# Kernel optimization log

Hardware: AMD Instinct MI355X
Metric: run time of the kernel (lower is better)

## Reference

```python
import jax, jax.numpy as jnp
import numpy as np


def _lstm_step(h, c, x, W_ih, W_hh, b_ih, b_hh):
    # PyTorch gate order: i, f, g, o
    gates = x @ W_ih.T + b_ih + h @ W_hh.T + b_hh
    i, f, g, o = jnp.split(gates, 4, axis=-1)
    c = jax.nn.sigmoid(f) * c + jax.nn.sigmoid(i) * jnp.tanh(g)
    h = jax.nn.sigmoid(o) * jnp.tanh(c)
    return h, c


def setup_inputs() -> dict:
    key = jax.random.key(0)
    ks = jax.random.split(key, 12)
    B, T = 256, 256
    S, A, H, K = 64, 16, 512, 512
    D = S + A  # 80
    s = 1.0 / np.sqrt(H)
    u = lambda k, shape, sc: jax.random.uniform(k, shape, jnp.float32, -sc, sc)
    return {
        "traj": jax.random.normal(ks[0], (B, T, D), jnp.float32),
        "seq_len": T,
        "enc_W_ih": u(ks[1], (4 * H, D), s),
        "enc_W_hh": u(ks[2], (4 * H, H), s),
        "enc_b_ih": u(ks[3], (4 * H,), s),
        "enc_b_hh": u(ks[4], (4 * H,), s),
        "embeddings": jax.random.uniform(ks[5], (K, H), jnp.float32, -1.0 / K, 1.0 / K),
        "dec_W_ih": u(ks[6], (4 * H, D), s),
        "dec_W_hh": u(ks[7], (4 * H, H), s),
        "dec_b_ih": u(ks[8], (4 * H,), s),
        "dec_b_hh": u(ks[9], (4 * H,), s),
        "fc_W": u(ks[10], (D, H), s),
        "fc_b": u(ks[11], (D,), s),
    }


def reference(traj, seq_len, enc_W_ih, enc_W_hh, enc_b_ih, enc_b_hh,
              embeddings, dec_W_ih, dec_W_hh, dec_b_ih, dec_b_hh, fc_W, fc_b):
    B = traj.shape[0]
    H = enc_W_hh.shape[1]
    D = traj.shape[-1]

    # ---- Encoder: many-to-one LSTM, keep final hidden state ----
    def enc_step(carry, x_t):
        h, c = carry
        h, c = _lstm_step(h, c, x_t, enc_W_ih, enc_W_hh, enc_b_ih, enc_b_hh)
        return (h, c), None
    h0 = jnp.zeros((B, H), traj.dtype)
    (z, _), _ = jax.lax.scan(enc_step, (h0, h0), jnp.swapaxes(traj, 0, 1))

    # ---- Vector quantizer ----
    d = (jnp.sum(z * z, axis=1, keepdims=True)
         + jnp.sum(embeddings * embeddings, axis=1)
         - 2.0 * z @ embeddings.T)  # [B, K]
    idx = jnp.argmin(d, axis=1)
    quantized = embeddings[idx]  # [B, H]
    e_latent = jnp.mean((jax.lax.stop_gradient(quantized) - z) ** 2)
    q_latent = jnp.mean((quantized - jax.lax.stop_gradient(z)) ** 2)
    vq_loss = q_latent + 0.25 * e_latent

    def dec_step(carry, _):
        h, c, x = carry
        h, c = _lstm_step(h, c, x, dec_W_ih, dec_W_hh, dec_b_ih, dec_b_hh)
        y = h @ fc_W.T + fc_b
        return (h, c, y), y
    x0 = jnp.zeros((B, D), traj.dtype)
    c0 = jnp.zeros((B, H), traj.dtype)
    _, ys = jax.lax.scan(dec_step, (quantized, c0, x0), None, length=seq_len)
    recon = jnp.swapaxes(ys, 0, 1)  # [B, seq_len, D]
    return recon, vq_loss, idx[:, None]
```

## Files before the change

kernel.cpp:

```cpp
#include <hip/hip_runtime.h>
#include <math.h>

#define BB 256
#define TT 256
#define DDIM 80
#define HDIM 512
#define ROWSTRIDE 20480

#define WS_HA    0
#define WS_CD    131072
#define WS_BAR   262144
#define WS_HB    263168
#define WS_QUANT 394240
#define WS_VQP   525312
#define WS_BENC  525568
#define WS_BDEC0 527616
#define WS_BEFF  529664
#define WS_WEFF  531712

typedef _Float16 f16;
typedef f16 half4_t __attribute__((ext_vector_type(4)));
typedef f16 half8_t __attribute__((ext_vector_type(8)));
typedef float float4_t __attribute__((ext_vector_type(4)));

__device__ __forceinline__ float sigmoid_fast(float v) {
  return __builtin_amdgcn_rcpf(1.0f + __builtin_amdgcn_exp2f(-1.44269504f * v));
}
__device__ __forceinline__ float tanh_fast(float v) {
  return 2.0f * __builtin_amdgcn_rcpf(1.0f + __builtin_amdgcn_exp2f(-2.88539008f * v)) - 1.0f;
}

__device__ __forceinline__ void llc_store_f32(float* p, float v) {
  asm volatile("global_store_dword %0, %1, off sc0 sc1" :: "v"(p), "v"(v) : "memory");
}
__device__ __forceinline__ void llc_store_i32(int* p, int v) {
  asm volatile("global_store_dword %0, %1, off sc0 sc1" :: "v"(p), "v"(v) : "memory");
}
__device__ __forceinline__ void wait_vm0() {
  asm volatile("s_waitcnt vmcnt(0)" ::: "memory");
}

__device__ __forceinline__ void poll_flag4(const int* fp, int done) {
  int a0, a1, a2, a3;
  asm volatile(
      "global_load_dword %0, %4, off sc0 sc1\n\t"
      "global_load_dword %1, %4, off sc0 sc1\n\t"
      "global_load_dword %2, %4, off sc0 sc1\n\t"
      "Lpoll%=:\n\t"
      "global_load_dword %3, %4, off sc0 sc1\n\t"
      "s_waitcnt vmcnt(3)\n\t"
      "v_cmp_gt_i32 vcc, %5, %0\n\t"
      "s_cbranch_vccz Ldone%=\n\t"
      "global_load_dword %0, %4, off sc0 sc1\n\t"
      "s_waitcnt vmcnt(3)\n\t"
      "v_cmp_gt_i32 vcc, %5, %1\n\t"
      "s_cbranch_vccz Ldone%=\n\t"
      "global_load_dword %1, %4, off sc0 sc1\n\t"
      "s_waitcnt vmcnt(3)\n\t"
      "v_cmp_gt_i32 vcc, %5, %2\n\t"
      "s_cbranch_vccz Ldone%=\n\t"
      "global_load_dword %2, %4, off sc0 sc1\n\t"
      "s_waitcnt vmcnt(3)\n\t"
      "v_cmp_gt_i32 vcc, %5, %3\n\t"
      "s_cbranch_vccnz Lpoll%=\n\t"
      "Ldone%=:\n\t"
      "s_waitcnt vmcnt(0)"
      : "=&v"(a0), "=&v"(a1), "=&v"(a2), "=&v"(a3)
      : "v"(fp), "s"(done)
      : "vcc", "memory");
}

__device__ __forceinline__ void llc_load_4xf4_cols(
    const float4* base,
    float4& a0, float4& a1, float4& a2, float4& a3) {
  asm volatile(
      "global_load_dwordx4 %0, %4, off sc0 sc1\n\t"
      "global_load_dwordx4 %1, %5, off sc0 sc1\n\t"
      "global_load_dwordx4 %2, %6, off sc0 sc1\n\t"
      "global_load_dwordx4 %3, %7, off sc0 sc1\n\t"
      "s_waitcnt vmcnt(0)"
      : "=&v"(a0), "=&v"(a1), "=&v"(a2), "=&v"(a3)
      : "v"(base), "v"(base + 32), "v"(base + 64), "v"(base + 96)
      : "memory");
}

__global__ __launch_bounds__(256) void zero_kernel(float4* __restrict__ p, int n4) {
  int i = blockIdx.x * 256 + threadIdx.x;
  if (i < n4) p[i] = make_float4(0.f, 0.f, 0.f, 0.f);
}

__global__ __launch_bounds__(256) void bias_init_kernel(
    const float* __restrict__ eb1, const float* __restrict__ eb2,
    const float* __restrict__ db1, const float* __restrict__ db2,
    const float* __restrict__ dWih, const float* __restrict__ fcb,
    float* __restrict__ b_enc, float* __restrict__ b_dec0,
    float* __restrict__ b_eff) {
  int n = blockIdx.x * 256 + threadIdx.x;
  b_enc[n] = eb1[n] + eb2[n];
  float bd = db1[n] + db2[n];
  b_dec0[n] = bd;
  float acc = bd;
  #pragma unroll 16
  for (int d = 0; d < DDIM; d++) acc += dWih[n * DDIM + d] * fcb[d];
  b_eff[n] = acc;
}

__global__ __launch_bounds__(256) void fold_kernel(
    const float* __restrict__ dWih, const float* __restrict__ dWhh,
    const float* __restrict__ fcW, float* __restrict__ W_eff) {
  int n = blockIdx.x;
  int tid = threadIdx.x;
  __shared__ float sw[DDIM];
  if (tid < DDIM) sw[tid] = dWih[n * DDIM + tid];
  __syncthreads();
  for (int k = tid; k < HDIM; k += 256) {
    float acc = dWhh[n * HDIM + k];
    #pragma unroll 16
    for (int d = 0; d < DDIM; d++) acc += sw[d] * fcW[d * HDIM + k];
    W_eff[n * HDIM + k] = acc;
  }
}

__global__ __launch_bounds__(256) void lstm_step_kernel(
    const float* __restrict__ Whh, const float* __restrict__ bias,
    const float* __restrict__ h_in, float* __restrict__ c,
    float* __restrict__ h_out) {
  __shared__ float sh[16][516];
  int tid = threadIdx.x;
  int rt = blockIdx.x & 15, jt = blockIdx.x >> 4;
  int row0 = rt << 4;
  for (int i = tid; i < 2048; i += 256) {
    int r = i >> 7, kq = i & 127;
    float4 v = *(const float4*)(h_in + (size_t)(row0 + r) * HDIM + (kq << 2));
    *(float4*)&sh[r][kq << 2] = v;
  }
  __syncthreads();
  int r = tid & 15, j0 = tid >> 4;
  int j = (jt << 4) + j0;
  float a0 = bias[j], a1 = bias[512 + j], a2 = bias[1024 + j], a3 = bias[1536 + j];
  const float4* w0 = (const float4*)(Whh + (size_t)j * HDIM);
  const float4* w1 = (const float4*)(Whh + (size_t)(512 + j) * HDIM);
  const float4* w2 = (const float4*)(Whh + (size_t)(1024 + j) * HDIM);
  const float4* w3 = (const float4*)(Whh + (size_t)(1536 + j) * HDIM);
  const float4* hv = (const float4*)&sh[r][0];
  #pragma unroll 4
  for (int kq = 0; kq < 128; kq++) {
    float4 h4 = hv[kq];
    float4 q0 = w0[kq], q1 = w1[kq], q2 = w2[kq], q3 = w3[kq];
    a0 += h4.x * q0.x + h4.y * q0.y + h4.z * q0.z + h4.w * q0.w;
    a1 += h4.x * q1.x + h4.y * q1.y + h4.z * q1.z + h4.w * q1.w;
    a2 += h4.x * q2.x + h4.y * q2.y + h4.z * q2.z + h4.w * q2.w;
    a3 += h4.x * q3.x + h4.y * q3.y + h4.z * q3.z + h4.w * q3.w;
  }
  size_t idx = (size_t)(row0 + r) * HDIM + j;
  float cv = c[idx];
  float cn = sigmoid_fast(a1) * cv + sigmoid_fast(a0) * tanh_fast(a2);
  float hn = sigmoid_fast(a3) * tanh_fast(cn);
  c[idx] = cn;
  h_out[idx] = hn;
}

template <int IS_DEC>
__global__ __launch_bounds__(512, 2) void lstm_persist(
    const float* __restrict__ W,
    const float* __restrict__ Wih,
    const float* __restrict__ bias,
    const float* __restrict__ traj,
    const float* __restrict__ c_init,
    const float* __restrict__ fcW, const float* __restrict__ fcb,
    float* __restrict__ recon,
    float* __restrict__ hA, float* __restrict__ hB,
    int* __restrict__ flags) {
  constexpr int KT  = IS_DEC ? 16 : 19;
  constexpr int AST = IS_DEC ? 520 : 616;
  constexpr int RST = 132;
  __shared__ f16 Ahi[16 * AST];
  __shared__ f16 Alo[16 * AST];
  __shared__ float red[16 * RST];
  __shared__ float ypart[IS_DEC ? 8 * 260 : 4];

  const int tid = threadIdx.x;
  const int bid = blockIdx.x;
  const int rt = bid & 15, jt = bid >> 4;
  const int r0 = rt * 16, d0 = jt * 32;
  const int wv = __builtin_amdgcn_readfirstlane(tid >> 6);
  const int l15 = tid & 15;
  const int q = (tid >> 4) & 3;
  const int dh = wv >> 2, nt = wv & 3;

  #define SPLITC(vv, k) { \
    int off = (tid >> 5) * AST + (((tid & 31) + (k) * 32) << 2); \
    half4_t hi4, lo4; \
    float f0 = vv.x, f1 = vv.y, f2 = vv.z, f3 = vv.w; \
    f16 a = (f16)f0, b = (f16)f1, cc = (f16)f2, d = (f16)f3; \
    hi4[0] = a; hi4[1] = b; hi4[2] = cc; hi4[3] = d; \
    lo4[0] = (f16)(f0 - (float)a); lo4[1] = (f16)(f1 - (float)b); \
    lo4[2] = (f16)(f2 - (float)cc); lo4[3] = (f16)(f3 - (float)d); \
    *(half4_t*)&Ahi[off] = hi4; *(half4_t*)&Alo[off] = lo4; }

  const int grow = nt * 512 + d0 + dh * 16 + l15;
  half8_t Whi[KT], Wlo[KT];
  #pragma unroll
  for (int kt = 0; kt < KT; kt++) {
    #pragma unroll
    for (int j = 0; j < 8; j++) {
      int k = kt * 32 + q * 8 + j;
      float w;
      if (k < 512) w = W[(size_t)grow * HDIM + k];
      else {
        int kx = k - 512;
        w = (!IS_DEC && kx < DDIM) ? Wih[(size_t)grow * DDIM + kx] : 0.f;
      }
      f16 hi = (f16)w;
      Whi[kt][j] = hi;
      Wlo[kt][j] = (f16)(w - (float)hi);
    }
  }
  const float breg = bias[grow];

  half8_t Fhi[2], Flo[2];
  float ybias = 0.f;
  if (IS_DEC && jt < 5) {
    const int drow = jt * 16 + l15;
    #pragma unroll
    for (int kk = 0; kk < 2; kk++) {
      const int kt = wv * 2 + kk;
      #pragma unroll
      for (int j = 0; j < 8; j++) {
        float w = fcW[(size_t)drow * HDIM + kt * 32 + q * 8 + j];
        f16 hi = (f16)w;
        Fhi[kk][j] = hi;
        Flo[kk][j] = (f16)(w - (float)hi);
      }
    }
    ybias = fcb[jt * 16 + l15];
  }

  const int eb = tid >> 5, ed = tid & 31;
  float c_reg = IS_DEC ? c_init[(size_t)(r0 + eb) * HDIM + d0 + ed] : 0.f;
  __syncthreads();

  #define MFMA_RANGE(LO, HI) { \
    _Pragma("unroll") \
    for (int kt = (LO); kt < (HI); kt++) { \
      half8_t ahi = *(const half8_t*)&Ahi[abase + kt * 32]; \
      half8_t alo = *(const half8_t*)&Alo[abase + kt * 32]; \
      if (kt & 1) { \
        acc1 = __builtin_amdgcn_mfma_f32_16x16x32_f16(ahi, Whi[kt], acc1, 0, 0, 0); \
        acc1 = __builtin_amdgcn_mfma_f32_16x16x32_f16(alo, Whi[kt], acc1, 0, 0, 0); \
        acc1 = __builtin_amdgcn_mfma_f32_16x16x32_f16(ahi, Wlo[kt], acc1, 0, 0, 0); \
        acc1 = __builtin_amdgcn_mfma_f32_16x16x32_f16(alo, Wlo[kt], acc1, 0, 0, 0); \
      } else { \
        acc0 = __builtin_amdgcn_mfma_f32_16x16x32_f16(ahi, Whi[kt], acc0, 0, 0, 0); \
        acc0 = __builtin_amdgcn_mfma_f32_16x16x32_f16(alo, Whi[kt], acc0, 0, 0, 0); \
        acc0 = __builtin_amdgcn_mfma_f32_16x16x32_f16(ahi, Wlo[kt], acc0, 0, 0, 0); \
        acc0 = __builtin_amdgcn_mfma_f32_16x16x32_f16(alo, Wlo[kt], acc0, 0, 0, 0); \
      } \
    } }

  const int t_begin = IS_DEC ? 1 : 0;
  for (int t = t_begin; t < TT; t++) {
    const float* hin = (t & 1) ? hB : hA;
    float* hout = (t & 1) ? hA : hB;

    float4 xv0;
    if (!IS_DEC && tid < 384) {
      int row = tid / 24, c4 = tid % 24;
      xv0 = (c4 < 20)
          ? *(const float4*)(traj + (size_t)(r0 + row) * ROWSTRIDE +
                             (size_t)t * DDIM + c4 * 4)
          : make_float4(0.f, 0.f, 0.f, 0.f);
    }

    float4 v0, v1, v2, v3;
    const float4* base =
        (const float4*)(hin + (size_t)r0 * HDIM) + (tid >> 5) * 128 + (tid & 31);
    const bool is_t0 = (!IS_DEC && t == 0);
    if (!is_t0) {
      asm volatile(
          "global_load_dwordx4 %0, %4, off sc0 sc1\n\t"
          "global_load_dwordx4 %1, %5, off sc0 sc1\n\t"
          "global_load_dwordx4 %2, %6, off sc0 sc1\n\t"
          "global_load_dwordx4 %3, %7, off sc0 sc1"
          : "=&v"(v0), "=&v"(v1), "=&v"(v2), "=&v"(v3)
          : "v"(base), "v"(base + 32), "v"(base + 64), "v"(base + 96)
          : "memory");
      asm volatile("s_waitcnt vmcnt(2)" ::: "memory");
      __builtin_amdgcn_sched_barrier(0);
      SPLITC(v0, 0); SPLITC(v1, 1);
    } else {
      const int fo = (tid >> 5) * AST + ((tid & 31) << 4);
      uint4 z4; z4.x = 0; z4.y = 0; z4.z = 0; z4.w = 0;
      *(uint4*)&Ahi[fo] = z4; *(uint4*)&Ahi[fo + 8] = z4;
      *(uint4*)&Alo[fo] = z4; *(uint4*)&Alo[fo + 8] = z4;
    }
    __syncthreads();

    float4_t acc0 = {breg, breg, breg, breg};
    float4_t acc1 = {0.f, 0.f, 0.f, 0.f};
    const int abase = l15 * AST + q * 8;
    MFMA_RANGE(0, 8);

    if (!is_t0) {
      asm volatile("s_waitcnt vmcnt(0)" ::: "memory");
      __builtin_amdgcn_sched_barrier(0);
      SPLITC(v2, 2); SPLITC(v3, 3);
    }
    if (!IS_DEC && tid < 384) {
      int row = tid / 24, c4 = tid % 24;
      int off = row * AST + 512 + c4 * 4;
      half4_t hi4, lo4;
      float f0 = xv0.x, f1 = xv0.y, f2 = xv0.z, f3 = xv0.w;
      f16 a = (f16)f0, b = (f16)f1, cc = (f16)f2, d = (f16)f3;
      hi4[0] = a; hi4[1] = b; hi4[2] = cc; hi4[3] = d;
      lo4[0] = (f16)(f0 - (float)a); lo4[1] = (f16)(f1 - (float)b);
      lo4[2] = (f16)(f2 - (float)cc); lo4[3] = (f16)(f3 - (float)d);
      *(half4_t*)&Ahi[off] = hi4; *(half4_t*)&Alo[off] = lo4;
    }
    __syncthreads();
    MFMA_RANGE(8, KT);
    {
      float4_t C = acc0 + acc1;
      #pragma unroll
      for (int i = 0; i < 4; i++)
        red[(q * 4 + i) * RST + nt * 32 + dh * 16 + l15] = C[i];
    }
    __syncthreads();

    {
      float ig = red[eb * RST + ed];
      float fg = red[eb * RST + 32 + ed];
      float gg = red[eb * RST + 64 + ed];
      float og = red[eb * RST + 96 + ed];
      float cn = sigmoid_fast(fg) * c_reg + sigmoid_fast(ig) * tanh_fast(gg);
      c_reg = cn;
      llc_store_f32(&hout[(size_t)(r0 + eb) * HDIM + d0 + ed],
                    sigmoid_fast(og) * tanh_fast(cn));
    }
    wait_vm0();
    __syncthreads();

    const int done = t - t_begin + 1;
    const bool do_bar = IS_DEC || t < TT - 1;
    if (do_bar && tid == 0) llc_store_i32(&flags[rt * 16 + jt], done);

    if (IS_DEC && jt < 5) {
      float4_t ya = {0.f, 0.f, 0.f, 0.f};
      #pragma unroll
      for (int kk = 0; kk < 2; kk++) {
        const int kt = wv * 2 + kk;
        const int ao = l15 * AST + kt * 32 + q * 8;
        half8_t ahi = *(const half8_t*)&Ahi[ao];
        half8_t alo = *(const half8_t*)&Alo[ao];
        ya = __builtin_amdgcn_mfma_f32_16x16x32_f16(ahi, Fhi[kk], ya, 0, 0, 0);
        ya = __builtin_amdgcn_mfma_f32_16x16x32_f16(alo, Fhi[kk], ya, 0, 0, 0);
        ya = __builtin_amdgcn_mfma_f32_16x16x32_f16(ahi, Flo[kk], ya, 0, 0, 0);
        ya = __builtin_amdgcn_mfma_f32_16x16x32_f16(alo, Flo[kk], ya, 0, 0, 0);
      }
      #pragma unroll
      for (int i = 0; i < 4; i++)
        ypart[wv * 260 + (q * 4 + i) * 16 + l15] = ya[i];
      __syncthreads();
      if (tid < 256) {
        float acc = ybias;
        #pragma unroll
        for (int w8 = 0; w8 < 8; w8++) acc += ypart[w8 * 260 + tid];
        recon[(size_t)(r0 + (tid >> 4)) * ROWSTRIDE + (size_t)(t - 1) * DDIM +
              jt * 16 + (tid & 15)] = acc;
      }
    }

    if (do_bar) {
      if (tid < 64) poll_flag4(flags + rt * 16 + (tid & 15), done);
      __syncthreads();
    }
  }

  if (IS_DEC) {
    if (jt >= 5) return;
    {
      const float4* base =
          (const float4*)(hA + (size_t)r0 * HDIM) + (tid >> 5) * 128 + (tid & 31);
      float4 v0, v1, v2, v3;
      llc_load_4xf4_cols(base, v0, v1, v2, v3);
      __builtin_amdgcn_sched_barrier(0);
      SPLITC(v0, 0); SPLITC(v1, 1); SPLITC(v2, 2); SPLITC(v3, 3);
    }
    __syncthreads();
    {
      float4_t ya = {0.f, 0.f, 0.f, 0.f};
      #pragma unroll
      for (int kk = 0; kk < 2; kk++) {
        const int kt = wv * 2 + kk;
        const int ao = l15 * AST + kt * 32 + q * 8;
        half8_t ahi = *(const half8_t*)&Ahi[ao];
        half8_t alo = *(const half8_t*)&Alo[ao];
        ya = __builtin_amdgcn_mfma_f32_16x16x32_f16(ahi, Fhi[kk], ya, 0, 0, 0);
        ya = __builtin_amdgcn_mfma_f32_16x16x32_f16(alo, Fhi[kk], ya, 0, 0, 0);
        ya = __builtin_amdgcn_mfma_f32_16x16x32_f16(ahi, Flo[kk], ya, 0, 0, 0);
        ya = __builtin_amdgcn_mfma_f32_16x16x32_f16(alo, Flo[kk], ya, 0, 0, 0);
      }
      #pragma unroll
      for (int i = 0; i < 4; i++)
        ypart[wv * 260 + (q * 4 + i) * 16 + l15] = ya[i];
    }
    __syncthreads();
    if (tid < 256) {
      float acc = ybias;
      #pragma unroll
      for (int w8 = 0; w8 < 8; w8++) acc += ypart[w8 * 260 + tid];
      recon[(size_t)(r0 + (tid >> 4)) * ROWSTRIDE + (size_t)255 * DDIM +
            jt * 16 + (tid & 15)] = acc;
    }
  }
  #undef SPLITC
  #undef MFMA_RANGE
}

__global__ __launch_bounds__(256) void vq_kernel(
    const float* __restrict__ z, const float* __restrict__ emb,
    float* __restrict__ quant, float* __restrict__ vq_part,
    float* __restrict__ out_idx) {
  __shared__ float sz[512];
  __shared__ float sd[256];
  __shared__ int si[256];
  int b = blockIdx.x, tid = threadIdx.x;
  sz[tid] = z[(size_t)b * HDIM + tid];
  sz[tid + 256] = z[(size_t)b * HDIM + 256 + tid];
  __syncthreads();
  float bd = 3.4e38f;
  int bk = 0;
  for (int k = tid; k < 512; k += 256) {
    const float4* e4 = (const float4*)(emb + (size_t)k * HDIM);
    const float4* z4 = (const float4*)sz;
    float dot = 0.f, ee = 0.f;
    #pragma unroll 4
    for (int qq = 0; qq < 128; qq++) {
      float4 ev = e4[qq], zv = z4[qq];
      dot += ev.x * zv.x + ev.y * zv.y + ev.z * zv.z + ev.w * zv.w;
      ee += ev.x * ev.x + ev.y * ev.y + ev.z * ev.z + ev.w * ev.w;
    }
    float dist = ee - 2.f * dot;
    if (dist < bd) { bd = dist; bk = k; }
  }
  sd[tid] = bd; si[tid] = bk;
  __syncthreads();
  for (int s = 128; s > 0; s >>= 1) {
    if (tid < s) {
      float od = sd[tid + s]; int ok = si[tid + s];
      if (od < sd[tid] || (od == sd[tid] && ok < si[tid])) { sd[tid] = od; si[tid] = ok; }
    }
    __syncthreads();
  }
  int kbest = si[0];
  __syncthreads();
  float e0 = emb[(size_t)kbest * HDIM + tid];
  float e1 = emb[(size_t)kbest * HDIM + 256 + tid];
  quant[(size_t)b * HDIM + tid] = e0;
  quant[(size_t)b * HDIM + 256 + tid] = e1;
  float q0 = e0 - sz[tid], q1 = e1 - sz[tid + 256];
  sd[tid] = q0 * q0 + q1 * q1;
  __syncthreads();
  for (int st = 128; st > 0; st >>= 1) {
    if (tid < st) sd[tid] += sd[tid + st];
    __syncthreads();
  }
  if (tid == 0) { vq_part[b] = sd[0]; out_idx[b] = (float)kbest; }
}

__global__ __launch_bounds__(256) void vq_reduce_kernel(const float* __restrict__ vq_part,
                                                        float* __restrict__ out_loss) {
  __shared__ float s[256];
  int tid = threadIdx.x;
  s[tid] = vq_part[tid];
  __syncthreads();
  for (int st = 128; st > 0; st >>= 1) {
    if (tid < st) s[tid] += s[tid + st];
    __syncthreads();
  }
  if (tid == 0) out_loss[0] = s[0] * 1.25f / (float)(BB * HDIM);
}

extern "C" void kernel_launch(void* const* d_in, const int* in_sizes, int n_in,
                              void* d_out, int out_size, void* d_ws, size_t ws_size,
                              hipStream_t stream) {
  const float* traj = (const float*)d_in[0];
  const float* eWih = (const float*)d_in[2];
  const float* eWhh = (const float*)d_in[3];
  const float* eb1  = (const float*)d_in[4];
  const float* eb2  = (const float*)d_in[5];
  const float* emb  = (const float*)d_in[6];
  const float* dWih = (const float*)d_in[7];
  const float* dWhh = (const float*)d_in[8];
  const float* db1  = (const float*)d_in[9];
  const float* db2  = (const float*)d_in[10];
  const float* fcW  = (const float*)d_in[11];
  const float* fcb  = (const float*)d_in[12];

  float* out = (float*)d_out;
  float* recon = out;
  float* out_loss = out + 5242880;
  float* out_idx = out + 5242881;

  float* ws = (float*)d_ws;
  float* hA      = ws + WS_HA;
  float* cD      = ws + WS_CD;
  int*   bar     = (int*)(ws + WS_BAR);
  float* hB      = ws + WS_HB;
  float* quant   = ws + WS_QUANT;
  float* vq_part = ws + WS_VQP;
  float* b_enc   = ws + WS_BENC;
  float* b_dec0  = ws + WS_BDEC0;
  float* b_eff   = ws + WS_BEFF;
  float* W_eff   = ws + WS_WEFF;

  zero_kernel<<<257, 256, 0, stream>>>((float4*)ws, 65792);
  bias_init_kernel<<<8, 256, 0, stream>>>(eb1, eb2, db1, db2, dWih, fcb,
                                          b_enc, b_dec0, b_eff);
  fold_kernel<<<2048, 256, 0, stream>>>(dWih, dWhh, fcW, W_eff);

  lstm_persist<0><<<256, 512, 0, stream>>>(
      eWhh, eWih, b_enc, traj, nullptr, nullptr, nullptr, nullptr, hA, hB, bar);

  vq_kernel<<<256, 256, 0, stream>>>(hA, emb, quant, vq_part, out_idx);
  vq_reduce_kernel<<<1, 256, 0, stream>>>(vq_part, out_loss);

  lstm_step_kernel<<<512, 256, 0, stream>>>(dWhh, b_dec0, quant, cD, hB);
  lstm_persist<1><<<256, 512, 0, stream>>>(
      W_eff, nullptr, b_eff, nullptr, cD, fcW, fcb, recon, hA, hB, bar + 256);
}
```

Measured before the change: 1.973 ms.

## Double per-block hidden slice in persistent LSTM, halving blocks and barrier fan-in

The persistent encoder and decoder LSTM kernels are relaunched as 128 blocks of 1024 threads instead of 256 blocks of 512, so each block owns 64 hidden columns instead of 32. The h-tile staging, gate reduction buffer, fc projection split and flag layout are reworked to match, so each row group now synchronises 8 blocks per step instead of 16. This is meant to cut the cross-block barrier cost on each recurrent step. The risk is register pressure: 1024-thread blocks (and the aggressive launch bounds) limit per-thread registers, and spilling the register-resident weight tiles could outweigh the sync savings.

```diff
diff --git a/kernel.cpp b/kernel.cpp
--- a/kernel.cpp
+++ b/kernel.cpp
@@ -70,20 +70,6 @@
       : "vcc", "memory");
 }
 
-__device__ __forceinline__ void llc_load_4xf4_cols(
-    const float4* base,
-    float4& a0, float4& a1, float4& a2, float4& a3) {
-  asm volatile(
-      "global_load_dwordx4 %0, %4, off sc0 sc1\n\t"
-      "global_load_dwordx4 %1, %5, off sc0 sc1\n\t"
-      "global_load_dwordx4 %2, %6, off sc0 sc1\n\t"
-      "global_load_dwordx4 %3, %7, off sc0 sc1\n\t"
-      "s_waitcnt vmcnt(0)"
-      : "=&v"(a0), "=&v"(a1), "=&v"(a2), "=&v"(a3)
-      : "v"(base), "v"(base + 32), "v"(base + 64), "v"(base + 96)
-      : "memory");
-}
-
 __global__ __launch_bounds__(256) void zero_kernel(float4* __restrict__ p, int n4) {
   int i = blockIdx.x * 256 + threadIdx.x;
   if (i < n4) p[i] = make_float4(0.f, 0.f, 0.f, 0.f);
@@ -161,7 +147,7 @@
 }
 
 template <int IS_DEC>
-__global__ __launch_bounds__(512, 2) void lstm_persist(
+__global__ __launch_bounds__(1024, 4) void lstm_persist(
     const float* __restrict__ W,
     const float* __restrict__ Wih,
     const float* __restrict__ bias,
@@ -173,23 +159,23 @@
     int* __restrict__ flags) {
   constexpr int KT  = IS_DEC ? 16 : 19;
   constexpr int AST = IS_DEC ? 520 : 616;
-  constexpr int RST = 132;
+  constexpr int RST = 260;
   __shared__ f16 Ahi[16 * AST];
   __shared__ f16 Alo[16 * AST];
   __shared__ float red[16 * RST];
-  __shared__ float ypart[IS_DEC ? 8 * 260 : 4];
+  __shared__ float ypart[IS_DEC ? 16 * 260 : 4];
 
   const int tid = threadIdx.x;
   const int bid = blockIdx.x;
   const int rt = bid & 15, jt = bid >> 4;
-  const int r0 = rt * 16, d0 = jt * 32;
+  const int r0 = rt * 16, d0 = jt * 64;
   const int wv = __builtin_amdgcn_readfirstlane(tid >> 6);
   const int l15 = tid & 15;
   const int q = (tid >> 4) & 3;
-  const int dh = wv >> 2, nt = wv & 3;
+  const int nt = wv & 3, dq = wv >> 2;
 
   #define SPLITC(vv, k) { \
-    int off = (tid >> 5) * AST + (((tid & 31) + (k) * 32) << 2); \
+    int off = (tid >> 6) * AST + (((tid & 63) + (k) * 64) << 2); \
     half4_t hi4, lo4; \
     float f0 = vv.x, f1 = vv.y, f2 = vv.z, f3 = vv.w; \
     f16 a = (f16)f0, b = (f16)f1, cc = (f16)f2, d = (f16)f3; \
@@ -198,7 +184,7 @@
     lo4[2] = (f16)(f2 - (float)cc); lo4[3] = (f16)(f3 - (float)d); \
     *(half4_t*)&Ahi[off] = hi4; *(half4_t*)&Alo[off] = lo4; }
 
-  const int grow = nt * 512 + d0 + dh * 16 + l15;
+  const int grow = nt * 512 + d0 + dq * 16 + l15;
   half8_t Whi[KT], Wlo[KT];
   #pragma unroll
   for (int kt = 0; kt < KT; kt++) {
@@ -218,25 +204,21 @@
   }
   const float breg = bias[grow];
 
-  half8_t Fhi[2], Flo[2];
+  half8_t Fhi, Flo;
   float ybias = 0.f;
   if (IS_DEC && jt < 5) {
     const int drow = jt * 16 + l15;
     #pragma unroll
-    for (int kk = 0; kk < 2; kk++) {
-      const int kt = wv * 2 + kk;
-      #pragma unroll
-      for (int j = 0; j < 8; j++) {
-        float w = fcW[(size_t)drow * HDIM + kt * 32 + q * 8 + j];
-        f16 hi = (f16)w;
-        Fhi[kk][j] = hi;
-        Flo[kk][j] = (f16)(w - (float)hi);
-      }
+    for (int j = 0; j < 8; j++) {
+      float w = fcW[(size_t)drow * HDIM + wv * 32 + q * 8 + j];
+      f16 hi = (f16)w;
+      Fhi[j] = hi;
+      Flo[j] = (f16)(w - (float)hi);
     }
     ybias = fcb[jt * 16 + l15];
   }
 
-  const int eb = tid >> 5, ed = tid & 31;
+  const int eb = tid >> 6, ed = tid & 63;
   float c_reg = IS_DEC ? c_init[(size_t)(r0 + eb) * HDIM + d0 + ed] : 0.f;
   __syncthreads();
 
@@ -272,27 +254,25 @@
           : make_float4(0.f, 0.f, 0.f, 0.f);
     }
 
-    float4 v0, v1, v2, v3;
+    float4 v0, v1;
     const float4* base =
-        (const float4*)(hin + (size_t)r0 * HDIM) + (tid >> 5) * 128 + (tid & 31);
+        (const float4*)(hin + (size_t)r0 * HDIM) + (tid >> 6) * 128 + (tid & 63);
     const bool is_t0 = (!IS_DEC && t == 0);
     if (!is_t0) {
       asm volatile(
-          "global_load_dwordx4 %0, %4, off sc0 sc1\n\t"
-          "global_load_dwordx4 %1, %5, off sc0 sc1\n\t"
-          "global_load_dwordx4 %2, %6, off sc0 sc1\n\t"
-          "global_load_dwordx4 %3, %7, off sc0 sc1"
-          : "=&v"(v0), "=&v"(v1), "=&v"(v2), "=&v"(v3)
-          : "v"(base), "v"(base + 32), "v"(base + 64), "v"(base + 96)
+          "global_load_dwordx4 %0, %2, off sc0 sc1\n\t"
+          "global_load_dwordx4 %1, %3, off sc0 sc1"
+          : "=&v"(v0), "=&v"(v1)
+          : "v"(base), "v"(base + 64)
           : "memory");
-      asm volatile("s_waitcnt vmcnt(2)" ::: "memory");
+      asm volatile("s_waitcnt vmcnt(1)" ::: "memory");
       __builtin_amdgcn_sched_barrier(0);
-      SPLITC(v0, 0); SPLITC(v1, 1);
+      SPLITC(v0, 0);
     } else {
-      const int fo = (tid >> 5) * AST + ((tid & 31) << 4);
-      uint4 z4; z4.x = 0; z4.y = 0; z4.z = 0; z4.w = 0;
-      *(uint4*)&Ahi[fo] = z4; *(uint4*)&Ahi[fo + 8] = z4;
-      *(uint4*)&Alo[fo] = z4; *(uint4*)&Alo[fo + 8] = z4;
+      const int fo = (tid >> 6) * AST + ((tid & 63) << 2);
+      half4_t z4 = {(f16)0, (f16)0, (f16)0, (f16)0};
+      *(half4_t*)&Ahi[fo] = z4; *(half4_t*)&Ahi[fo + 256] = z4;
+      *(half4_t*)&Alo[fo] = z4; *(half4_t*)&Alo[fo + 256] = z4;
     }
     __syncthreads();
 
@@ -304,7 +284,7 @@
     if (!is_t0) {
       asm volatile("s_waitcnt vmcnt(0)" ::: "memory");
       __builtin_amdgcn_sched_barrier(0);
-      SPLITC(v2, 2); SPLITC(v3, 3);
+      SPLITC(v1, 1);
     }
     if (!IS_DEC && tid < 384) {
       int row = tid / 24, c4 = tid % 24;
@@ -323,15 +303,15 @@
       float4_t C = acc0 + acc1;
       #pragma unroll
       for (int i = 0; i < 4; i++)
-        red[(q * 4 + i) * RST + nt * 32 + dh * 16 + l15] = C[i];
+        red[(q * 4 + i) * RST + nt * 64 + dq * 16 + l15] = C[i];
     }
     __syncthreads();
 
     {
       float ig = red[eb * RST + ed];
-      float fg = red[eb * RST + 32 + ed];
-      float gg = red[eb * RST + 64 + ed];
-      float og = red[eb * RST + 96 + ed];
+      float fg = red[eb * RST + 64 + ed];
+      float gg = red[eb * RST + 128 + ed];
+      float og = red[eb * RST + 192 + ed];
       float cn = sigmoid_fast(fg) * c_reg + sigmoid_fast(ig) * tanh_fast(gg);
       c_reg = cn;
       llc_store_f32(&hout[(size_t)(r0 + eb) * HDIM + d0 + ed],
@@ -342,20 +322,18 @@
 
     const int done = t - t_begin + 1;
     const bool do_bar = IS_DEC || t < TT - 1;
-    if (do_bar && tid == 0) llc_store_i32(&flags[rt * 16 + jt], done);
+    if (do_bar && tid == 0) llc_store_i32(&flags[rt * 8 + jt], done);
 
     if (IS_DEC && jt < 5) {
       float4_t ya = {0.f, 0.f, 0.f, 0.f};
-      #pragma unroll
-      for (int kk = 0; kk < 2; kk++) {
-        const int kt = wv * 2 + kk;
-        const int ao = l15 * AST + kt * 32 + q * 8;
+      {
+        const int ao = l15 * AST + wv * 32 + q * 8;
         half8_t ahi = *(const half8_t*)&Ahi[ao];
         half8_t alo = *(const half8_t*)&Alo[ao];
-        ya = __builtin_amdgcn_mfma_f32_16x16x32_f16(ahi, Fhi[kk], ya, 0, 0, 0);
-        ya = __builtin_amdgcn_mfma_f32_16x16x32_f16(alo, Fhi[kk], ya, 0, 0, 0);
-        ya = __builtin_amdgcn_mfma_f32_16x16x32_f16(ahi, Flo[kk], ya, 0, 0, 0);
-        ya = __builtin_amdgcn_mfma_f32_16x16x32_f16(alo, Flo[kk], ya, 0, 0, 0);
+        ya = __builtin_amdgcn_mfma_f32_16x16x32_f16(ahi, Fhi, ya, 0, 0, 0);
+        ya = __builtin_amdgcn_mfma_f32_16x16x32_f16(alo, Fhi, ya, 0, 0, 0);
+        ya = __builtin_amdgcn_mfma_f32_16x16x32_f16(ahi, Flo, ya, 0, 0, 0);
+        ya = __builtin_amdgcn_mfma_f32_16x16x32_f16(alo, Flo, ya, 0, 0, 0);
       }
       #pragma unroll
       for (int i = 0; i < 4; i++)
@@ -364,14 +342,14 @@
       if (tid < 256) {
         float acc = ybias;
         #pragma unroll
-        for (int w8 = 0; w8 < 8; w8++) acc += ypart[w8 * 260 + tid];
+        for (int w16 = 0; w16 < 16; w16++) acc += ypart[w16 * 260 + tid];
         recon[(size_t)(r0 + (tid >> 4)) * ROWSTRIDE + (size_t)(t - 1) * DDIM +
               jt * 16 + (tid & 15)] = acc;
       }
     }
 
     if (do_bar) {
-      if (tid < 64) poll_flag4(flags + rt * 16 + (tid & 15), done);
+      if (tid < 64) poll_flag4(flags + rt * 8 + (tid & 7), done);
       __syncthreads();
     }
   }
@@ -380,25 +358,29 @@
     if (jt >= 5) return;
     {
       const float4* base =
-          (const float4*)(hA + (size_t)r0 * HDIM) + (tid >> 5) * 128 + (tid & 31);
-      float4 v0, v1, v2, v3;
-      llc_load_4xf4_cols(base, v0, v1, v2, v3);
+          (const float4*)(hA + (size_t)r0 * HDIM) + (tid >> 6) * 128 + (tid & 63);
+      float4 v0, v1;
+      asm volatile(
+          "global_load_dwordx4 %0, %2, off sc0 sc1\n\t"
+          "global_load_dwordx4 %1, %3, off sc0 sc1\n\t"
+          "s_waitcnt vmcnt(0)"
+          : "=&v"(v0), "=&v"(v1)
+          : "v"(base), "v"(base + 64)
+          : "memory");
       __builtin_amdgcn_sched_barrier(0);
-      SPLITC(v0, 0); SPLITC(v1, 1); SPLITC(v2, 2); SPLITC(v3, 3);
+      SPLITC(v0, 0); SPLITC(v1, 1);
     }
     __syncthreads();
     {
       float4_t ya = {0.f, 0.f, 0.f, 0.f};
-      #pragma unroll
-      for (int kk = 0; kk < 2; kk++) {
-        const int kt = wv * 2 + kk;
-        const int ao = l15 * AST + kt * 32 + q * 8;
+      {
+        const int ao = l15 * AST + wv * 32 + q * 8;
         half8_t ahi = *(const half8_t*)&Ahi[ao];
         half8_t alo = *(const half8_t*)&Alo[ao];
-        ya = __builtin_amdgcn_mfma_f32_16x16x32_f16(ahi, Fhi[kk], ya, 0, 0, 0);
-        ya = __builtin_amdgcn_mfma_f32_16x16x32_f16(alo, Fhi[kk], ya, 0, 0, 0);
-        ya = __builtin_amdgcn_mfma_f32_16x16x32_f16(ahi, Flo[kk], ya, 0, 0, 0);
-        ya = __builtin_amdgcn_mfma_f32_16x16x32_f16(alo, Flo[kk], ya, 0, 0, 0);
+        ya = __builtin_amdgcn_mfma_f32_16x16x32_f16(ahi, Fhi, ya, 0, 0, 0);
+        ya = __builtin_amdgcn_mfma_f32_16x16x32_f16(alo, Fhi, ya, 0, 0, 0);
+        ya = __builtin_amdgcn_mfma_f32_16x16x32_f16(ahi, Flo, ya, 0, 0, 0);
+        ya = __builtin_amdgcn_mfma_f32_16x16x32_f16(alo, Flo, ya, 0, 0, 0);
       }
       #pragma unroll
       for (int i = 0; i < 4; i++)
@@ -408,7 +390,7 @@
     if (tid < 256) {
       float acc = ybias;
       #pragma unroll
-      for (int w8 = 0; w8 < 8; w8++) acc += ypart[w8 * 260 + tid];
+      for (int w16 = 0; w16 < 16; w16++) acc += ypart[w16 * 260 + tid];
       recon[(size_t)(r0 + (tid >> 4)) * ROWSTRIDE + (size_t)255 * DDIM +
             jt * 16 + (tid & 15)] = acc;
     }
@@ -519,13 +501,13 @@
                                           b_enc, b_dec0, b_eff);
   fold_kernel<<<2048, 256, 0, stream>>>(dWih, dWhh, fcW, W_eff);
 
-  lstm_persist<0><<<256, 512, 0, stream>>>(
+  lstm_persist<0><<<128, 1024, 0, stream>>>(
       eWhh, eWih, b_enc, traj, nullptr, nullptr, nullptr, nullptr, hA, hB, bar);
 
   vq_kernel<<<256, 256, 0, stream>>>(hA, emb, quant, vq_part, out_idx);
   vq_reduce_kernel<<<1, 256, 0, stream>>>(vq_part, out_loss);
 
   lstm_step_kernel<<<512, 256, 0, stream>>>(dWhh, b_dec0, quant, cD, hB);
-  lstm_persist<1><<<256, 512, 0, stream>>>(
+  lstm_persist<1><<<128, 1024, 0, stream>>>(
       W_eff, nullptr, b_eff, nullptr, cD, fcW, fcb, recon, hA, hB, bar + 256);
 }
```

After: 6.234 ms. +215.9%, slower.
